# Kernel tuning notes

Hardware: AMD Instinct MI355X
Metric: run time of the kernel (lower is better)

Reference implementation:

```python
import jax, jax.numpy as jnp
import numpy as np

B, D, NB, E, DT, K, TS = 16384, 512, 8, 4, 256, 8, 16
GH = max(D // 2, 16)            # gate hidden = 256
SH = max(int(DT * 0.5), 16)     # safe head hidden = 128
SPD = DT + TS                   # spec head input = 272
SPH = max(int(SPD * 0.25), 16)  # spec hidden = 68
CFD = DT + 1 + 3 + TS + 1 + 1   # conf input = 278
CFH = max(int(CFD * 0.25), 16)  # conf hidden = 69


def _ln(x, g, b):
    m = x.mean(-1, keepdims=True)
    v = ((x - m) ** 2).mean(-1, keepdims=True)
    return (x - m) / jnp.sqrt(v + 1e-5) * g + b


def _resmlp(x, lg, lb, W1, b1, W2, b2):
    h = jax.nn.relu(_ln(x, lg, lb) @ W1 + b1)
    return h @ W2 + b2


def setup_inputs() -> dict:
    key = jax.random.key(0)
    ks = iter(jax.random.split(key, 48))

    def n(shape, s=0.02):
        return (jax.random.normal(next(ks), shape, jnp.float32) * s).astype(jnp.float32)

    inp = {
        'x_num': jax.random.normal(next(ks), (B, D), jnp.float32),
        # GGPLNumericEmbedding
        'basis_weight': n((D, NB + 1, E), 0.001),
        'basis_bias': jnp.zeros((D, E), jnp.float32),
        'bp_min': jnp.zeros((D, 1), jnp.float32),
        'bp_delta_raw': n((D, NB), 0.1),
        'proj_W': n((D * E, D)), 'proj_b': jnp.zeros((D,), jnp.float32),
        # input gate MLP
        'gate_W1': n((D, GH)), 'gate_b1': jnp.zeros((GH,), jnp.float32),
        'gate_W2': n((GH, D)), 'gate_b2': jnp.zeros((D,), jnp.float32),
        # backbone stand-in (TMLPBackbone.encode_hidden): 2-layer MLP -> d_token
        'bb_W1': n((D, DT)), 'bb_b1': jnp.zeros((DT,), jnp.float32),
        'bb_W2': n((DT, DT)), 'bb_b2': jnp.zeros((DT,), jnp.float32),
        # base head
        'base_W': n((DT, 1)), 'base_b': jnp.zeros((1,), jnp.float32),
        # safe residual head (zero_last=True -> zero last weight)
        'safe_ln_g': jnp.ones((DT,), jnp.float32), 'safe_ln_b': jnp.zeros((DT,), jnp.float32),
        'safe_W1': n((DT, SH)), 'safe_b1': jnp.zeros((SH,), jnp.float32),
        'safe_W2': jnp.zeros((SH, 1), jnp.float32), 'safe_b2': jnp.zeros((1,), jnp.float32),
        # top feature summary
        'top_W1': n((1, TS), 0.001), 'top_b1': jnp.zeros((TS,), jnp.float32),
        'top_W2': n((TS, TS), 0.001), 'top_b2': jnp.zeros((TS,), jnp.float32),
        # spec head
        'spec_ln_g': jnp.ones((SPD,), jnp.float32), 'spec_ln_b': jnp.zeros((SPD,), jnp.float32),
        'spec_W1': n((SPD, SPH)), 'spec_b1': jnp.zeros((SPH,), jnp.float32),
        'spec_W2': n((SPH, 1), 0.001), 'spec_b2': jnp.zeros((1,), jnp.float32),
        # conf gate (last bias init = -2.0)
        'conf_ln_g': jnp.ones((CFD,), jnp.float32), 'conf_ln_b': jnp.zeros((CFD,), jnp.float32),
        'conf_W1': n((CFD, CFH)), 'conf_b1': jnp.zeros((CFH,), jnp.float32),
        'conf_W2': n((CFH, 1), 0.001), 'conf_b2': jnp.full((1,), -2.0, jnp.float32),
    }
    return inp


def reference(x_num, basis_weight, basis_bias, bp_min, bp_delta_raw, proj_W, proj_b,
              gate_W1, gate_b1, gate_W2, gate_b2, bb_W1, bb_b1, bb_W2, bb_b2,
              base_W, base_b, safe_ln_g, safe_ln_b, safe_W1, safe_b1, safe_W2, safe_b2,
              top_W1, top_b1, top_W2, top_b2, spec_ln_g, spec_ln_b, spec_W1, spec_b1,
              spec_W2, spec_b2, conf_ln_g, conf_ln_b, conf_W1, conf_b1, conf_W2, conf_b2):
    # --- GGPL numeric embedding ---
    bps = bp_min + jnp.cumsum(jax.nn.softplus(bp_delta_raw), axis=1)        # [D, NB]
    basis = jnp.concatenate([x_num[..., None],
                             jax.nn.relu(x_num[..., None] - bps[None])], -1)  # [B, D, NB+1]
    emb = jnp.einsum('bdf,dfe->bde', basis, basis_weight) + basis_bias       # [B, D, E]
    flat = emb.reshape(x_num.shape[0], -1)
    x_in = x_num + 0.1 * (flat @ proj_W + proj_b)
    # --- input gate ---
    g = jax.nn.sigmoid(jax.nn.relu(x_in @ gate_W1 + gate_b1) @ gate_W2 + gate_b2)
    x_gated = x_in * g
    # --- backbone + base head ---
    h = jax.nn.relu(jax.nn.relu(x_gated @ bb_W1 + bb_b1) @ bb_W2 + bb_b2)    # [B, DT]
    y_base = h @ base_W + base_b                                             # [B, 1]
    # --- gate stats (population std, matching unbiased=False) ---
    gmean = g.mean(1, keepdims=True)
    gmax = g.max(1, keepdims=True)
    gstd = g.std(1, keepdims=True)
    # --- safe residual head ---
    delta_safe = _resmlp(h, safe_ln_g, safe_ln_b, safe_W1, safe_b1, safe_W2, safe_b2)
    # --- top-k gate selection + gather ---
    topk_g, topk_idx = jax.lax.top_k(g, K)                                   # [B, K]
    topk_x = jnp.take_along_axis(x_in, topk_idx, axis=1)
    topk_w = topk_g / (topk_g.sum(1, keepdims=True) + 1e-6)
    xw = (topk_x * topk_w)[..., None]                                        # [B, K, 1]
    tokens = jax.nn.relu(xw @ top_W1 + top_b1) @ top_W2 + top_b2             # [B, K, TS]
    z_top = tokens.mean(1)                                                   # [B, TS]
    # --- spec head + confidence gate ---
    delta_spec = _resmlp(jnp.concatenate([h, z_top], 1),
                         spec_ln_g, spec_ln_b, spec_W1, spec_b1, spec_W2, spec_b2)
    conf_in = jnp.concatenate([h, y_base, gmean, gmax, gstd, z_top,
                               jnp.abs(delta_safe), jnp.abs(delta_spec)], 1)
    gamma = jax.nn.sigmoid(_resmlp(conf_in, conf_ln_g, conf_ln_b,
                                   conf_W1, conf_b1, conf_W2, conf_b2))
    y_hat = y_base + delta_safe + gamma * delta_spec
    return y_hat.squeeze(-1)                                                 # [B]
```

## Files before the change

kernel.cpp:

```cpp
#include <hip/hip_runtime.h>
#include <cstddef>

typedef unsigned short u16;
typedef unsigned int   u32;
typedef short bf16x8 __attribute__((ext_vector_type(8)));
typedef float f32x4 __attribute__((ext_vector_type(4)));

#define B_ROWS 16384
#define D_FEAT 512
#define NB_    8

static __device__ __forceinline__ float b2f(u16 h) {
    union { u32 u; float f; } v; v.u = ((u32)h) << 16; return v.f;
}
static __device__ __forceinline__ u16 f2b(float f) {
    union { float f; u32 u; } v; v.f = f;
    u32 r = (v.u + 0x7fffu + ((v.u >> 16) & 1u)) >> 16;
    return (u16)r;
}
static __device__ __forceinline__ float ldf(const void* p, size_t i, int isb) {
    return isb ? b2f(((const u16*)p)[i]) : ((const float*)p)[i];
}
static __device__ __forceinline__ u16 cvtb(const void* p, size_t i, int isb) {
    return isb ? ((const u16*)p)[i] : f2b(((const float*)p)[i]);
}
static __device__ __forceinline__ float wred_sum(float v) {
    #pragma unroll
    for (int off = 32; off > 0; off >>= 1) v += __shfl_xor(v, off);
    return v;
}
static __device__ __forceinline__ float wred_max(float v) {
    #pragma unroll
    for (int off = 32; off > 0; off >>= 1) v = fmaxf(v, __shfl_xor(v, off));
    return v;
}
static __device__ __forceinline__ u32 umax2(u32 a, u32 b) { return a > b ? a : b; }
static __device__ __forceinline__ void async_copy16(const u16* g, u16* l) {
    __builtin_amdgcn_global_load_lds(
        (const __attribute__((address_space(1))) u32*)g,
        (__attribute__((address_space(3))) u32*)l, 16, 0, 0);
}
static __device__ __forceinline__ int detect_isb(const void* xnum) {
    int lane = threadIdx.x & 63;
    u16 h = ((const u16*)xnum)[lane * 2];
    int e = (h >> 7) & 0xff;
    unsigned long long m = __ballot(e >= 110 && e <= 132);
    return (__popcll(m) >= 32) ? 1 : 0;
}

#define WO_PROJ 0
#define WO_GW1  1048576
#define WO_GW2  1179648
#define WO_BW1  1310720
#define WO_BW2  1441792
#define WO_SW1  1507328
#define WO_SPW  1540096
#define WO_CFW  1581056
#define W_TOTAL 1622016

#define NB_TRANS 376
#define NB_SPW 160
struct PrepArgs {
    const void *xnum;
    const void *src[6];
    const void *spW, *cfW;
    const void *pb, *g1, *g2, *b1, *b2, *sb, *spb, *cfb;
    const void *bwt, *bbias, *bp_min, *bp_dr;
    u16 *Wbuf; float *biasbuf, *bwT, *bbT, *bpsT;
    int *flag;
};

__global__ __launch_bounds__(256) void prep_all_k(PrepArgs P) {
    __shared__ int s_isb;
    __shared__ u16 tile[64][68];
    if (threadIdx.x < 64) { int r = detect_isb(P.xnum); if ((threadIdx.x & 63) == 0) s_isb = r; }
    __syncthreads();
    const int isb = s_isb;
    const int tid = threadIdx.x;

    if (blockIdx.x < NB_TRANS) {
        const int Ks[6]   = {2048, 512, 256, 512, 256, 256};
        const int Nss[6]  = {512, 256, 512, 256, 256, 128};
        const int offs[6] = {WO_PROJ, WO_GW1, WO_GW2, WO_BW1, WO_BW2, WO_SW1};
        int bid = blockIdx.x, m = 0;
        #pragma unroll
        for (int i = 0; i < 6; ++i) {
            int nt = (Ks[i] >> 6) * (Nss[i] >> 6);
            if (bid >= nt && m == i) { bid -= nt; m = i + 1; }
        }
        const int K = Ks[m], N = Nss[m];
        const int ktiles = K >> 6;
        const int tn = bid / ktiles, tk = bid % ktiles;
        const int k0 = tk * 64, n0 = tn * 64;
        const void* src = P.src[m];
        u16* dst = P.Wbuf + offs[m];
        #pragma unroll
        for (int p = 0; p < 16; ++p) {
            int kk = p * 4 + (tid >> 6);
            int nn = tid & 63;
            tile[kk][nn] = cvtb(src, (size_t)(k0 + kk) * N + n0 + nn, isb);
        }
        __syncthreads();
        #pragma unroll
        for (int p = 0; p < 16; ++p) {
            int nn = p * 4 + (tid >> 6);
            int kk = tid & 63;
            dst[(size_t)(n0 + nn) * K + k0 + kk] = tile[kk][nn];
        }
        return;
    }

    const int bid = blockIdx.x - NB_TRANS;
    if (bid < NB_SPW) {
        size_t i = (size_t)bid * 256 + tid;
        int n = (int)(i / 320), k = (int)(i % 320);
        P.Wbuf[WO_SPW + i] =
            (n < 68 && k < 272) ? cvtb(P.spW, (size_t)k * 68 + n, isb) : (u16)0;
    } else if (bid < 2 * NB_SPW) {
        size_t i = (size_t)(bid - NB_SPW) * 256 + tid;
        int n = (int)(i / 320), k = (int)(i % 320);
        P.Wbuf[WO_CFW + i] =
            (n < 69 && k < 278) ? cvtb(P.cfW, (size_t)k * 69 + n, isb) : (u16)0;
    } else if (bid < 2 * NB_SPW + 9) {
        int t = (bid - 2 * NB_SPW) * 256 + tid;
        float* out = P.biasbuf;
        if      (t < 512)  out[t] = ldf(P.pb, t, isb);
        else if (t < 768)  out[t] = ldf(P.g1, t - 512, isb);
        else if (t < 1280) out[t] = ldf(P.g2, t - 768, isb);
        else if (t < 1536) out[t] = ldf(P.b1, t - 1280, isb);
        else if (t < 1792) out[t] = ldf(P.b2, t - 1536, isb);
        else if (t < 1920) out[t] = ldf(P.sb, t - 1792, isb);
        else if (t < 2048) { int c = t - 1920; out[t] = (c < 68) ? ldf(P.spb, c, isb) : 0.f; }
        else if (t < 2176) { int c = t - 2048; out[t] = (c < 69) ? ldf(P.cfb, c, isb) : 0.f; }
    } else if (bid < 2 * NB_SPW + 9 + 72) {
        int t = (bid - 2 * NB_SPW - 9) * 256 + tid;
        if (t < 512 * 36) {
            int d = t / 36, j = t % 36;
            P.bwT[j * 512 + d] = ldf(P.bwt, t, isb);
        }
        if (t < 2048) {
            int d = t >> 2, e = t & 3;
            P.bbT[e * 512 + d] = ldf(P.bbias, t, isb);
        }
    } else {
        int d = (bid - 2 * NB_SPW - 9 - 72) * 256 + tid;
        if (d < D_FEAT) {
            float bp = ldf(P.bp_min, d, isb);
            #pragma unroll
            for (int k = 0; k < NB_; ++k) {
                float x = ldf(P.bp_dr, d * NB_ + k, isb);
                bp += fmaxf(x, 0.f) + log1pf(expf(-fabsf(x)));
                P.bpsT[k * 512 + d] = bp;
            }
        }
        if (d == 0) *P.flag = isb;
    }
}

__global__ __launch_bounds__(256) void emb_k(
    const void* __restrict__ xnum, const float* __restrict__ bwT,
    const float* __restrict__ bbT, const float* __restrict__ bpsT,
    u16* __restrict__ emb, const int* __restrict__ flag, int rowoff)
{
    const int isb = *flag;
    size_t gi = ((size_t)blockIdx.x * 256 + threadIdx.x) * 4;
    int d0 = (int)(gi & 511);
    float xv[4];
    if (isb) {
        u16 tmp[4];
        *(uint2*)tmp = *(const uint2*)((const u16*)xnum + (size_t)rowoff * 512 + gi);
        #pragma unroll
        for (int i = 0; i < 4; ++i) xv[i] = b2f(tmp[i]);
    } else {
        float4 f = *(const float4*)((const float*)xnum + (size_t)rowoff * 512 + gi);
        xv[0] = f.x; xv[1] = f.y; xv[2] = f.z; xv[3] = f.w;
    }
    float acc[4][4];
    #pragma unroll
    for (int e = 0; e < 4; ++e) {
        float4 b = *(const float4*)&bbT[e * 512 + d0];
        acc[0][e] = b.x; acc[1][e] = b.y; acc[2][e] = b.z; acc[3][e] = b.w;
    }
    #pragma unroll
    for (int f = 0; f <= 8; ++f) {
        float bv[4];
        if (f == 0) {
            #pragma unroll
            for (int i = 0; i < 4; ++i) bv[i] = xv[i];
        } else {
            float4 bp = *(const float4*)&bpsT[(f - 1) * 512 + d0];
            bv[0] = fmaxf(xv[0] - bp.x, 0.f); bv[1] = fmaxf(xv[1] - bp.y, 0.f);
            bv[2] = fmaxf(xv[2] - bp.z, 0.f); bv[3] = fmaxf(xv[3] - bp.w, 0.f);
        }
        #pragma unroll
        for (int e = 0; e < 4; ++e) {
            float4 w = *(const float4*)&bwT[(f * 4 + e) * 512 + d0];
            acc[0][e] = fmaf(bv[0], w.x, acc[0][e]);
            acc[1][e] = fmaf(bv[1], w.y, acc[1][e]);
            acc[2][e] = fmaf(bv[2], w.z, acc[2][e]);
            acc[3][e] = fmaf(bv[3], w.w, acc[3][e]);
        }
    }
    u16 o[16];
    #pragma unroll
    for (int i = 0; i < 4; ++i)
        #pragma unroll
        for (int e = 0; e < 4; ++e) o[i * 4 + e] = f2b(acc[i][e]);
    *(uint4*)&emb[gi * 4]     = *(const uint4*)&o[0];
    *(uint4*)&emb[gi * 4 + 8] = *(const uint4*)&o[8];
}

template<int EMODE>
__global__ __launch_bounds__(256) void mgemm_k(
    const u16* __restrict__ A, const u16* __restrict__ Bt,
    const float* __restrict__ bias,
    void* __restrict__ out0, const void* __restrict__ aux0, void* __restrict__ aux1,
    int N, int Kdim, int lda, int ldk, int rowoff, const int* __restrict__ flagp)
{
    __shared__ __align__(16) u16 As[2][64][64];
    __shared__ __align__(16) u16 Bs[2][64][64];

    const int isb = (EMODE == 0) ? *flagp : 0;
    const int tid = threadIdx.x;

    const int lin = blockIdx.y * gridDim.x + blockIdx.x;
    const int xc = lin & 7, ii = lin >> 3;
    const int ny = gridDim.y;
    const int row0 = (xc + 8 * (ii / ny)) * 64;
    const int col0 = (ii % ny) * 64;

    const int w = tid >> 6, lane = tid & 63, q = lane >> 4, mr = lane & 15;
    const int wr = (w >> 1) * 32, wc = (w & 1) * 32;
    const int rr = lane >> 3, kg = lane & 7;
    const int sc = kg ^ (rr & 7);

    f32x4 acc[2][2];
    #pragma unroll
    for (int a = 0; a < 2; ++a)
        #pragma unroll
        for (int b = 0; b < 2; ++b) acc[a][b] = (f32x4){0.f, 0.f, 0.f, 0.f};

    const int T = Kdim >> 6;

    auto stage = [&](int kt, int bi) {
        if (w < 2) {
            #pragma unroll
            for (int j = 0; j < 4; ++j) {
                int m = w * 32 + j * 8;
                async_copy16(A + (size_t)(row0 + m + rr) * lda + kt + sc * 8,
                             &As[bi][m][0]);
            }
        } else {
            #pragma unroll
            for (int j = 0; j < 4; ++j) {
                int m = (w - 2) * 32 + j * 8;
                async_copy16(Bt + (size_t)(col0 + m + rr) * ldk + kt + sc * 8,
                             &Bs[bi][m][0]);
            }
        }
    };

    stage(0, 0);
    __syncthreads();

    for (int t = 0; t < T; ++t) {
        if (t + 1 < T) stage((t + 1) << 6, (t + 1) & 1);
        const int cb = t & 1;
        #pragma unroll
        for (int ks = 0; ks < 2; ++ks) {
            bf16x8 af[2], bf[2];
            #pragma unroll
            for (int rs = 0; rs < 2; ++rs) {
                int r = wr + rs * 16 + mr;
                int pc = (ks * 4 + q) ^ (r & 7);
                af[rs] = *(const bf16x8*)&As[cb][r][pc * 8];
            }
            #pragma unroll
            for (int nt = 0; nt < 2; ++nt) {
                int r = wc + nt * 16 + mr;
                int pc = (ks * 4 + q) ^ (r & 7);
                bf[nt] = *(const bf16x8*)&Bs[cb][r][pc * 8];
            }
            #pragma unroll
            for (int rs = 0; rs < 2; ++rs)
                #pragma unroll
                for (int nt = 0; nt < 2; ++nt)
                    acc[rs][nt] = __builtin_amdgcn_mfma_f32_16x16x32_bf16(
                        af[rs], bf[nt], acc[rs][nt], 0, 0, 0);
        }
        __syncthreads();
    }

    #pragma unroll
    for (int rs = 0; rs < 2; ++rs) {
        #pragma unroll
        for (int i = 0; i < 4; ++i) {
            size_t gr = (size_t)rowoff + row0 + wr + rs * 16 + q * 4 + i;
            #pragma unroll
            for (int nt = 0; nt < 2; ++nt) {
                int c = col0 + wc + nt * 16 + mr;
                float z = acc[rs][nt][i] + bias[c];
                size_t idx = gr * (size_t)N + c;
                if (EMODE == 0) {
                    ((u16*)out0)[idx] = f2b(ldf(aux0, idx, isb) + 0.1f * z);
                } else if (EMODE == 1) {
                    ((u16*)out0)[idx] = f2b(fmaxf(z, 0.f));
                } else {
                    float gv = 1.f / (1.f + expf(-z));
                    ((u16*)out0)[idx] = f2b(gv);
                    ((u16*)aux1)[idx] = f2b(b2f(((const u16*)aux0)[idx]) * gv);
                }
            }
        }
    }
}

__global__ __launch_bounds__(256) void mgemm_pair_k(
    const u16* __restrict__ A1, const u16* __restrict__ B1,
    const float* __restrict__ bias1, u16* __restrict__ out1,
    int K1, int lda1, int ldk1,
    const u16* __restrict__ A2, const u16* __restrict__ B2,
    const float* __restrict__ bias2, u16* __restrict__ out2,
    int K2, int lda2, int ldk2,
    int N, int nx1)
{
    __shared__ __align__(16) u16 As[2][64][64];
    __shared__ __align__(16) u16 Bs[2][64][64];

    const int tid = threadIdx.x;
    const bool sec = blockIdx.x >= nx1;
    const u16* A = sec ? A2 : A1;
    const u16* Bt = sec ? B2 : B1;
    const float* bias = sec ? bias2 : bias1;
    u16* out0 = sec ? out2 : out1;
    const int Kdim = sec ? K2 : K1;
    const int lda = sec ? lda2 : lda1;
    const int ldk = sec ? ldk2 : ldk1;
    const int row0 = (sec ? blockIdx.x - nx1 : blockIdx.x) * 64;
    const int col0 = blockIdx.y * 64;
    const int w = tid >> 6, lane = tid & 63, q = lane >> 4, mr = lane & 15;
    const int wr = (w >> 1) * 32, wc = (w & 1) * 32;
    const int rr = lane >> 3, kg = lane & 7;
    const int sc = kg ^ (rr & 7);

    f32x4 acc[2][2];
    #pragma unroll
    for (int a = 0; a < 2; ++a)
        #pragma unroll
        for (int b = 0; b < 2; ++b) acc[a][b] = (f32x4){0.f, 0.f, 0.f, 0.f};

    const int T = Kdim >> 6;

    auto stage = [&](int kt, int bi) {
        if (w < 2) {
            #pragma unroll
            for (int j = 0; j < 4; ++j) {
                int m = w * 32 + j * 8;
                async_copy16(A + (size_t)(row0 + m + rr) * lda + kt + sc * 8,
                             &As[bi][m][0]);
            }
        } else {
            #pragma unroll
            for (int j = 0; j < 4; ++j) {
                int m = (w - 2) * 32 + j * 8;
                async_copy16(Bt + (size_t)(col0 + m + rr) * ldk + kt + sc * 8,
                             &Bs[bi][m][0]);
            }
        }
    };

    stage(0, 0);
    __syncthreads();

    for (int t = 0; t < T; ++t) {
        if (t + 1 < T) stage((t + 1) << 6, (t + 1) & 1);
        const int cb = t & 1;
        #pragma unroll
        for (int ks = 0; ks < 2; ++ks) {
            bf16x8 af[2], bf[2];
            #pragma unroll
            for (int rs = 0; rs < 2; ++rs) {
                int r = wr + rs * 16 + mr;
                int pc = (ks * 4 + q) ^ (r & 7);
                af[rs] = *(const bf16x8*)&As[cb][r][pc * 8];
            }
            #pragma unroll
            for (int nt = 0; nt < 2; ++nt) {
                int r = wc + nt * 16 + mr;
                int pc = (ks * 4 + q) ^ (r & 7);
                bf[nt] = *(const bf16x8*)&Bs[cb][r][pc * 8];
            }
            #pragma unroll
            for (int rs = 0; rs < 2; ++rs)
                #pragma unroll
                for (int nt = 0; nt < 2; ++nt)
                    acc[rs][nt] = __builtin_amdgcn_mfma_f32_16x16x32_bf16(
                        af[rs], bf[nt], acc[rs][nt], 0, 0, 0);
        }
        __syncthreads();
    }

    #pragma unroll
    for (int rs = 0; rs < 2; ++rs) {
        #pragma unroll
        for (int i = 0; i < 4; ++i) {
            size_t gr = (size_t)row0 + wr + rs * 16 + q * 4 + i;
            #pragma unroll
            for (int nt = 0; nt < 2; ++nt) {
                int c = col0 + wc + nt * 16 + mr;
                float z = acc[rs][nt][i] + bias[c];
                out0[gr * (size_t)N + c] = f2b(fmaxf(z, 0.f));
            }
        }
    }
}

struct PreArgs {
    const u16 *x_in, *g, *h;
    const void *base_W, *base_b;
    const void *safe_ln_g, *safe_ln_b;
    const void *top_W1, *top_b1, *top_W2, *top_b2;
    const void *spec_ln_g, *spec_ln_b;
    u16 *ln_a, *ln_b;
    float *scal;
    const int *flag;
};

__global__ __launch_bounds__(256, 4) void pre_k(PreArgs P) {
    __shared__ float w_base[256], w_slg[256], w_slb[256], w_t2[256];
    __shared__ float w_plg[272], w_plb[272];
    __shared__ float w_t1[16], w_tb1[16], w_tb2[16];
    const int isb = *P.flag;
    const int tid = threadIdx.x;
    const int wid = tid >> 6;
    const int lane = tid & 63;
    const int row = blockIdx.x * 4 + wid;

    w_base[tid] = ldf(P.base_W, tid, isb);
    w_slg[tid]  = ldf(P.safe_ln_g, tid, isb);
    w_slb[tid]  = ldf(P.safe_ln_b, tid, isb);
    w_t2[tid]   = ldf(P.top_W2, tid, isb);
    if (tid < 272) {
        w_plg[tid] = ldf(P.spec_ln_g, tid, isb);
        w_plb[tid] = ldf(P.spec_ln_b, tid, isb);
    }
    if (tid < 16) {
        w_t1[tid]  = ldf(P.top_W1, tid, isb);
        w_tb1[tid] = ldf(P.top_b1, tid, isb);
        w_tb2[tid] = ldf(P.top_b2, tid, isb);
    }
    __syncthreads();

    float hv[4], gv[8];
    u16 graw[8];
    #pragma unroll
    for (int i = 0; i < 4; ++i) hv[i] = b2f(P.h[(size_t)row * 256 + lane + 64 * i]);
    #pragma unroll
    for (int j = 0; j < 8; ++j) {
        graw[j] = P.g[(size_t)row * 512 + lane + 64 * j];
        gv[j] = b2f(graw[j]);
    }
    const float hsum = hv[0] + hv[1] + hv[2] + hv[3];

    float pb = 0.f;
    #pragma unroll
    for (int i = 0; i < 4; ++i) pb = fmaf(hv[i], w_base[lane + 64 * i], pb);
    const float yb = wred_sum(pb) + ldf(P.base_b, 0, isb);

    float s1 = 0.f, s2 = 0.f, mx = -1e30f;
    #pragma unroll
    for (int j = 0; j < 8; ++j) { s1 += gv[j]; s2 = fmaf(gv[j], gv[j], s2); mx = fmaxf(mx, gv[j]); }
    s1 = wred_sum(s1); s2 = wred_sum(s2); mx = wred_max(mx);
    const float gmean = s1 * (1.f / 512.f);
    const float gstd = sqrtf(fmaxf(s2 * (1.f / 512.f) - gmean * gmean, 0.f));

    const float hm = wred_sum(hsum) * (1.f / 256.f);
    float pv = 0.f;
    #pragma unroll
    for (int i = 0; i < 4; ++i) { float d = hv[i] - hm; pv = fmaf(d, d, pv); }
    const float hrstd = rsqrtf(wred_sum(pv) * (1.f / 256.f) + 1e-5f);
    #pragma unroll
    for (int i = 0; i < 4; ++i) {
        int k = lane + 64 * i;
        P.ln_a[(size_t)row * 320 + k] = f2b((hv[i] - hm) * hrstd * w_slg[k] + w_slb[k]);
    }

    u32 keys[8];
    #pragma unroll
    for (int j = 0; j < 8; ++j)
        keys[j] = ((u32)graw[j] << 9) | (u32)(511 - (lane + 64 * j));

    float myv = 0.f, sumtv = 0.f; int myi = 0;
    for (int r8 = 0; r8 < 8; ++r8) {
        u32 a = umax2(umax2(umax2(keys[0], keys[1]), umax2(keys[2], keys[3])),
                      umax2(umax2(keys[4], keys[5]), umax2(keys[6], keys[7])));
        #pragma unroll
        for (int off = 32; off > 0; off >>= 1)
            a = umax2(a, (u32)__shfl_xor((int)a, off));
        const int widx = 511 - (int)(a & 511u);
        const float wval = b2f((u16)(a >> 9));
        sumtv += wval;
        if (lane == r8) { myv = wval; myi = widx; }
        if ((widx & 63) == lane) {
            int oj = widx >> 6;
            #pragma unroll
            for (int j = 0; j < 8; ++j) if (j == oj) keys[j] = 0;
        }
    }

    float xw = 0.f;
    if (lane < 8) {
        float xi = b2f(P.x_in[(size_t)row * 512 + myi]);
        xw = xi * (myv / (sumtv + 1e-6f));
    }
    const int tt = lane & 15;
    float Sv = 0.f;
    #pragma unroll
    for (int k = 0; k < 8; ++k) {
        float xwk = __shfl(xw, k);
        Sv += fmaxf(fmaf(xwk, w_t1[tt], w_tb1[tt]), 0.f);
    }
    float zacc = w_tb2[tt];
    #pragma unroll
    for (int s = 0; s < 16; ++s)
        zacc = fmaf(__shfl(Sv, s), w_t2[s * 16 + tt], zacc);
    const float ztl = zacc * 0.125f;

    float ps = hsum + ((lane < 16) ? ztl : 0.f);
    const float sm = wred_sum(ps) * (1.f / 272.f);
    float pv2 = 0.f;
    #pragma unroll
    for (int i = 0; i < 4; ++i) { float d = hv[i] - sm; pv2 = fmaf(d, d, pv2); }
    if (lane < 16) { float d = ztl - sm; pv2 = fmaf(d, d, pv2); }
    const float srstd = rsqrtf(wred_sum(pv2) * (1.f / 272.f) + 1e-5f);
    #pragma unroll
    for (int i = 0; i < 4; ++i) {
        int k = lane + 64 * i;
        P.ln_b[(size_t)row * 320 + k] = f2b((hv[i] - sm) * srstd * w_plg[k] + w_plb[k]);
    }
    if (lane < 16) {
        int k = 256 + lane;
        P.ln_b[(size_t)row * 320 + k] = f2b((ztl - sm) * srstd * w_plg[k] + w_plb[k]);
    } else {
        P.ln_b[(size_t)row * 320 + 256 + lane] = 0;
    }

    float* sc = P.scal + (size_t)row * 32;
    if (lane < 16) sc[8 + lane] = ztl;
    if (lane == 0) { sc[0] = yb; sc[1] = gmean; sc[2] = mx; sc[3] = gstd; }
}

struct MidArgs {
    const u16 *h;
    const float *scal_in;
    const u16 *sh, *sph;
    const void *safe_W2, *safe_b2, *spec_W2, *spec_b2;
    const void *conf_ln_g, *conf_ln_b;
    u16 *ln_c;
    float *scal;
    const int *flag;
};

__global__ __launch_bounds__(256, 4) void mid_k(MidArgs P) {
    __shared__ float w_clg[278], w_clb[278], w_sw2[128], w_spw2[68];
    const int isb = *P.flag;
    const int tid = threadIdx.x;
    const int wid = tid >> 6;
    const int lane = tid & 63;
    const int row = blockIdx.x * 4 + wid;

    if (tid < 278) { w_clg[tid] = ldf(P.conf_ln_g, tid, isb); w_clb[tid] = ldf(P.conf_ln_b, tid, isb); }
    if (tid < 128) w_sw2[tid]  = ldf(P.safe_W2, tid, isb);
    if (tid < 68)  w_spw2[tid] = ldf(P.spec_W2, tid, isb);
    __syncthreads();

    float s0 = b2f(P.sh[(size_t)row * 128 + lane]);
    float s1 = b2f(P.sh[(size_t)row * 128 + 64 + lane]);
    float psafe = s0 * w_sw2[lane] + s1 * w_sw2[64 + lane];
    const float dsafe = wred_sum(psafe) + ldf(P.safe_b2, 0, isb);

    float p0 = b2f(P.sph[(size_t)row * 128 + lane]) * ((lane < 68) ? w_spw2[lane] : 0.f);
    if (lane < 4) p0 += b2f(P.sph[(size_t)row * 128 + 64 + lane]) * w_spw2[64 + lane];
    const float dspec = wred_sum(p0) + ldf(P.spec_b2, 0, isb);

    const float* sc = P.scal_in + (size_t)row * 32;
    const float yb = sc[0], gmean = sc[1], mx = sc[2], gstd = sc[3];
    const float ztl = (lane < 16) ? sc[8 + lane] : 0.f;

    float hv[4];
    #pragma unroll
    for (int i = 0; i < 4; ++i) hv[i] = b2f(P.h[(size_t)row * 256 + lane + 64 * i]);
    const float hsum = hv[0] + hv[1] + hv[2] + hv[3];

    const float ads = fabsf(dsafe), adsp = fabsf(dspec);
    float pc = hsum + ((lane < 16) ? ztl : 0.f)
             + ((lane == 0) ? (yb + gmean + mx + gstd + ads + adsp) : 0.f);
    const float cm = wred_sum(pc) * (1.f / 278.f);
    float pv3 = 0.f;
    #pragma unroll
    for (int i = 0; i < 4; ++i) { float d = hv[i] - cm; pv3 = fmaf(d, d, pv3); }
    if (lane < 16) { float d = ztl - cm; pv3 = fmaf(d, d, pv3); }
    if (lane == 0) {
        float vals[6] = { yb, gmean, mx, gstd, ads, adsp };
        #pragma unroll
        for (int q = 0; q < 6; ++q) { float d = vals[q] - cm; pv3 = fmaf(d, d, pv3); }
    }
    const float crstd = rsqrtf(wred_sum(pv3) * (1.f / 278.f) + 1e-5f);

    u16* la = P.ln_c + (size_t)row * 320;
    #pragma unroll
    for (int i = 0; i < 4; ++i) {
        int k = lane + 64 * i;
        la[k] = f2b((hv[i] - cm) * crstd * w_clg[k] + w_clb[k]);
    }
    if (lane < 16) {
        int k = 260 + lane;
        la[k] = f2b((ztl - cm) * crstd * w_clg[k] + w_clb[k]);
    } else if (lane >= 18 && lane < 60) {
        la[260 + lane] = 0;
    }
    if (lane == 0) {
        float vals[6] = { yb, gmean, mx, gstd, ads, adsp };
        int idxs[6] = { 256, 257, 258, 259, 276, 277 };
        #pragma unroll
        for (int q = 0; q < 6; ++q) {
            int k = idxs[q];
            la[k] = f2b((vals[q] - cm) * crstd * w_clg[k] + w_clb[k]);
        }
        float* so = P.scal + (size_t)row * 32;
        so[4] = dsafe; so[5] = dspec;
    }
}

__global__ __launch_bounds__(256, 4) void post_k(
    const u16* __restrict__ ch, const float* __restrict__ scal,
    const void* __restrict__ conf_W2, const void* __restrict__ conf_b2,
    void* __restrict__ out, const int* __restrict__ flag)
{
    __shared__ float w_cw2[69];
    const int isb = *flag;
    const int tid = threadIdx.x;
    const int wid = tid >> 6;
    const int lane = tid & 63;
    const int row = blockIdx.x * 4 + wid;

    if (tid < 69) w_cw2[tid] = ldf(conf_W2, tid, isb);
    __syncthreads();

    float c0 = b2f(ch[(size_t)row * 128 + lane]) * ((lane < 69) ? w_cw2[lane] : 0.f);
    if (lane < 5) c0 += b2f(ch[(size_t)row * 128 + 64 + lane]) * w_cw2[64 + lane];
    const float zlin = wred_sum(c0) + ldf(conf_b2, 0, isb);
    const float gamma = 1.f / (1.f + expf(-zlin));
    if (lane == 0) {
        const float* sc = scal + (size_t)row * 32;
        float v = sc[0] + sc[4] + gamma * sc[5];
        if (isb) ((u16*)out)[row] = f2b(v);
        else     ((float*)out)[row] = v;
    }
}

extern "C" void kernel_launch(void* const* d_in, const int* in_sizes, int n_in,
                              void* d_out, int out_size, void* d_ws, size_t ws_size,
                              hipStream_t stream) {
    (void)in_sizes; (void)n_in; (void)out_size; (void)ws_size;
    const void* x_num = d_in[0];

    char* p = (char*)d_ws;
    auto alloc = [&](size_t bytes) { char* r = p; p += (bytes + 15) & ~(size_t)15; return r; };

    int*   flag    = (int*)alloc(16);
    float* bpsT    = (float*)alloc(8 * 512 * 4);
    float* bwT     = (float*)alloc(36 * 512 * 4);
    float* bbT     = (float*)alloc(4 * 512 * 4);
    float* biasbuf = (float*)alloc(2176 * 4);
    u16*   Wbuf    = (u16*)alloc((size_t)W_TOTAL * 2);
    u16*   ebuf    = (u16*)alloc((size_t)(B_ROWS / 2) * 2048 * 2);
    u16*   x_in    = (u16*)alloc((size_t)B_ROWS * 512 * 2);
    u16*   hid1    = (u16*)alloc((size_t)B_ROWS * 256 * 2);
    u16*   hbuf    = (u16*)alloc((size_t)B_ROWS * 256 * 2);
    u16*   ln_a    = (u16*)alloc((size_t)B_ROWS * 320 * 2);
    u16*   ln_b    = (u16*)alloc((size_t)B_ROWS * 320 * 2);
    float* scal    = (float*)alloc((size_t)B_ROWS * 32 * 4);
    u16*   sh      = (u16*)alloc((size_t)B_ROWS * 128 * 2);
    u16*   sph     = (u16*)alloc((size_t)B_ROWS * 128 * 2);
    u16*   xg      = (u16*)alloc((size_t)B_ROWS * 512 * 2);
    u16*   hid2    = (u16*)alloc((size_t)B_ROWS * 256 * 2);

    u16*   g   = ebuf;
    u16*   chh = hid1;

    {
        PrepArgs pr;
        pr.xnum = x_num;
        pr.src[0] = d_in[5];  pr.src[1] = d_in[7];  pr.src[2] = d_in[9];
        pr.src[3] = d_in[11]; pr.src[4] = d_in[13]; pr.src[5] = d_in[19];
        pr.spW = d_in[29]; pr.cfW = d_in[35];
        pr.pb = d_in[6];  pr.g1 = d_in[8];  pr.g2 = d_in[10];
        pr.b1 = d_in[12]; pr.b2 = d_in[14]; pr.sb = d_in[20];
        pr.spb = d_in[30]; pr.cfb = d_in[36];
        pr.bwt = d_in[1]; pr.bbias = d_in[2];
        pr.bp_min = d_in[3]; pr.bp_dr = d_in[4];
        pr.Wbuf = Wbuf; pr.biasbuf = biasbuf;
        pr.bwT = bwT; pr.bbT = bbT; pr.bpsT = bpsT;
        pr.flag = flag;
        prep_all_k<<<NB_TRANS + 2 * NB_SPW + 9 + 72 + 2, 256, 0, stream>>>(pr);
    }

    const int HR = B_ROWS / 2;
    for (int half = 0; half < 2; ++half) {
        int rowoff = half * HR;
        emb_k<<<(HR * D_FEAT / 4) / 256, 256, 0, stream>>>(
            x_num, bwT, bbT, bpsT, ebuf, flag, rowoff);
        mgemm_k<0><<<dim3(HR / 64, 8), 256, 0, stream>>>(
            ebuf, Wbuf + WO_PROJ, biasbuf + 0, x_in, x_num, nullptr,
            512, 2048, 2048, 2048, rowoff, flag);
    }

    mgemm_k<1><<<dim3(B_ROWS / 64, 4), 256, 0, stream>>>(
        x_in, Wbuf + WO_GW1, biasbuf + 512, hid1, nullptr, nullptr,
        256, 512, 512, 512, 0, flag);
    mgemm_k<2><<<dim3(B_ROWS / 64, 8), 256, 0, stream>>>(
        hid1, Wbuf + WO_GW2, biasbuf + 768, g, x_in, xg,
        512, 256, 256, 256, 0, flag);
    mgemm_k<1><<<dim3(B_ROWS / 64, 4), 256, 0, stream>>>(
        xg, Wbuf + WO_BW1, biasbuf + 1280, hid2, nullptr, nullptr,
        256, 512, 512, 512, 0, flag);
    mgemm_k<1><<<dim3(B_ROWS / 64, 4), 256, 0, stream>>>(
        hid2, Wbuf + WO_BW2, biasbuf + 1536, hbuf, nullptr, nullptr,
        256, 256, 256, 256, 0, flag);

    {
        PreArgs pa;
        pa.x_in = x_in; pa.g = g; pa.h = hbuf;
        pa.base_W = d_in[15]; pa.base_b = d_in[16];
        pa.safe_ln_g = d_in[17]; pa.safe_ln_b = d_in[18];
        pa.top_W1 = d_in[23]; pa.top_b1 = d_in[24];
        pa.top_W2 = d_in[25]; pa.top_b2 = d_in[26];
        pa.spec_ln_g = d_in[27]; pa.spec_ln_b = d_in[28];
        pa.ln_a = ln_a; pa.ln_b = ln_b; pa.scal = scal; pa.flag = flag;
        pre_k<<<B_ROWS / 4, 256, 0, stream>>>(pa);
    }

    mgemm_pair_k<<<dim3(2 * (B_ROWS / 64), 2), 256, 0, stream>>>(
        ln_a, Wbuf + WO_SW1, biasbuf + 1792, sh, 256, 320, 256,
        ln_b, Wbuf + WO_SPW, biasbuf + 1920, sph, 320, 320, 320,
        128, B_ROWS / 64);

    {
        MidArgs ma;
        ma.h = hbuf; ma.scal_in = scal; ma.sh = sh; ma.sph = sph;
        ma.safe_W2 = d_in[21]; ma.safe_b2 = d_in[22];
        ma.spec_W2 = d_in[31]; ma.spec_b2 = d_in[32];
        ma.conf_ln_g = d_in[33]; ma.conf_ln_b = d_in[34];
        ma.ln_c = ln_a; ma.scal = scal; ma.flag = flag;
        mid_k<<<B_ROWS / 4, 256, 0, stream>>>(ma);
    }

    mgemm_k<1><<<dim3(B_ROWS / 64, 2), 256, 0, stream>>>(
        ln_a, Wbuf + WO_CFW, biasbuf + 2048, chh, nullptr, nullptr,
        128, 320, 320, 320, 0, flag);

    post_k<<<B_ROWS / 4, 256, 0, stream>>>(chh, scal, d_in[37], d_in[38], d_out, flag);
}
```

Measured before the change: 422.3 us.

## Add dedicated producer wave with triple-buffered LDS to mgemm kernel

```diff
diff --git a/kernel.cpp b/kernel.cpp
--- a/kernel.cpp
+++ b/kernel.cpp
@@ -211,14 +211,14 @@
 }
 
 template<int EMODE>
-__global__ __launch_bounds__(256) void mgemm_k(
+__global__ __launch_bounds__(320) void mgemm_k(
     const u16* __restrict__ A, const u16* __restrict__ Bt,
     const float* __restrict__ bias,
     void* __restrict__ out0, const void* __restrict__ aux0, void* __restrict__ aux1,
     int N, int Kdim, int lda, int ldk, int rowoff, const int* __restrict__ flagp)
 {
-    __shared__ __align__(16) u16 As[2][64][64];
-    __shared__ __align__(16) u16 Bs[2][64][64];
+    __shared__ __align__(16) u16 As[3][64][64];
+    __shared__ __align__(16) u16 Bs[3][64][64];
 
     const int isb = (EMODE == 0) ? *flagp : 0;
     const int tid = threadIdx.x;
@@ -230,42 +230,46 @@
     const int col0 = (ii % ny) * 64;
 
     const int w = tid >> 6, lane = tid & 63, q = lane >> 4, mr = lane & 15;
-    const int wr = (w >> 1) * 32, wc = (w & 1) * 32;
     const int rr = lane >> 3, kg = lane & 7;
     const int sc = kg ^ (rr & 7);
-
+    const int T = Kdim >> 6;
+
+    if (w == 4) {
+        auto stageP = [&](int kt, int bi) {
+            #pragma unroll
+            for (int j = 0; j < 8; ++j)
+                async_copy16(A + (size_t)(row0 + j * 8 + rr) * lda + kt + sc * 8,
+                             &As[bi][j * 8][0]);
+            #pragma unroll
+            for (int j = 0; j < 8; ++j)
+                async_copy16(Bt + (size_t)(col0 + j * 8 + rr) * ldk + kt + sc * 8,
+                             &Bs[bi][j * 8][0]);
+        };
+        stageP(0, 0);
+        stageP(64, 1);
+        int nb = 2;
+        for (int t = 0; t < T; ++t) {
+            if (t + 1 < T) __builtin_amdgcn_s_waitcnt(0x4F70);
+            else           __builtin_amdgcn_s_waitcnt(0x0F70);
+            __builtin_amdgcn_s_barrier();
+            if (t + 2 < T) {
+                stageP((t + 2) << 6, nb);
+                nb = (nb == 2) ? 0 : nb + 1;
+            }
+        }
+        return;
+    }
+
+    const int wr = (w >> 1) * 32, wc = (w & 1) * 32;
     f32x4 acc[2][2];
     #pragma unroll
     for (int a = 0; a < 2; ++a)
         #pragma unroll
         for (int b = 0; b < 2; ++b) acc[a][b] = (f32x4){0.f, 0.f, 0.f, 0.f};
 
-    const int T = Kdim >> 6;
-
-    auto stage = [&](int kt, int bi) {
-        if (w < 2) {
-            #pragma unroll
-            for (int j = 0; j < 4; ++j) {
-                int m = w * 32 + j * 8;
-                async_copy16(A + (size_t)(row0 + m + rr) * lda + kt + sc * 8,
-                             &As[bi][m][0]);
-            }
-        } else {
-            #pragma unroll
-            for (int j = 0; j < 4; ++j) {
-                int m = (w - 2) * 32 + j * 8;
-                async_copy16(Bt + (size_t)(col0 + m + rr) * ldk + kt + sc * 8,
-                             &Bs[bi][m][0]);
-            }
-        }
-    };
-
-    stage(0, 0);
-    __syncthreads();
-
+    int cb = 0;
     for (int t = 0; t < T; ++t) {
-        if (t + 1 < T) stage((t + 1) << 6, (t + 1) & 1);
-        const int cb = t & 1;
+        __syncthreads();
         #pragma unroll
         for (int ks = 0; ks < 2; ++ks) {
             bf16x8 af[2], bf[2];
@@ -288,7 +292,7 @@
                     acc[rs][nt] = __builtin_amdgcn_mfma_f32_16x16x32_bf16(
                         af[rs], bf[nt], acc[rs][nt], 0, 0, 0);
         }
-        __syncthreads();
+        cb = (cb == 2) ? 0 : cb + 1;
     }
 
     #pragma unroll
@@ -711,21 +715,21 @@
         int rowoff = half * HR;
         emb_k<<<(HR * D_FEAT / 4) / 256, 256, 0, stream>>>(
             x_num, bwT, bbT, bpsT, ebuf, flag, rowoff);
-        mgemm_k<0><<<dim3(HR / 64, 8), 256, 0, stream>>>(
+        mgemm_k<0><<<dim3(HR / 64, 8), 320, 0, stream>>>(
             ebuf, Wbuf + WO_PROJ, biasbuf + 0, x_in, x_num, nullptr,
             512, 2048, 2048, 2048, rowoff, flag);
     }
 
-    mgemm_k<1><<<dim3(B_ROWS / 64, 4), 256, 0, stream>>>(
+    mgemm_k<1><<<dim3(B_ROWS / 64, 4), 320, 0, stream>>>(
         x_in, Wbuf + WO_GW1, biasbuf + 512, hid1, nullptr, nullptr,
         256, 512, 512, 512, 0, flag);
-    mgemm_k<2><<<dim3(B_ROWS / 64, 8), 256, 0, stream>>>(
+    mgemm_k<2><<<dim3(B_ROWS / 64, 8), 320, 0, stream>>>(
         hid1, Wbuf + WO_GW2, biasbuf + 768, g, x_in, xg,
         512, 256, 256, 256, 0, flag);
-    mgemm_k<1><<<dim3(B_ROWS / 64, 4), 256, 0, stream>>>(
+    mgemm_k<1><<<dim3(B_ROWS / 64, 4), 320, 0, stream>>>(
         xg, Wbuf + WO_BW1, biasbuf + 1280, hid2, nullptr, nullptr,
         256, 512, 512, 512, 0, flag);
-    mgemm_k<1><<<dim3(B_ROWS / 64, 4), 256, 0, stream>>>(
+    mgemm_k<1><<<dim3(B_ROWS / 64, 4), 320, 0, stream>>>(
         hid2, Wbuf + WO_BW2, biasbuf + 1536, hbuf, nullptr, nullptr,
         256, 256, 256, 256, 0, flag);
 
@@ -756,7 +760,7 @@
         mid_k<<<B_ROWS / 4, 256, 0, stream>>>(ma);
     }
 
-    mgemm_k<1><<<dim3(B_ROWS / 64, 2), 256, 0, stream>>>(
+    mgemm_k<1><<<dim3(B_ROWS / 64, 2), 320, 0, stream>>>(
         ln_a, Wbuf + WO_CFW, biasbuf + 2048, chh, nullptr, nullptr,
         128, 320, 320, 320, 0, flag);
 
```

Measured after the change: 439.1 us. 1.04x slower.
